# Kernel tuning notes

Measured on AMD Instinct MI355X. Metric: run time of the kernel, lower is better.

## Reference

```python
import jax, jax.numpy as jnp
import numpy as np

N, E = 20000, 320000
IN_DIM = OUT_DIM = E_IN = E_OUT = 128
BN_EPS = 1e-5

def _lrelu(x):
    return jnp.where(x >= 0, x, 0.1 * x)

def setup_inputs() -> dict:
    key = jax.random.key(0)
    ks = jax.random.split(key, 12)
    def w(k, shape):
        return jax.random.normal(k, shape, jnp.float32) * (shape[0] ** -0.5)
    return {
        "h": jax.random.normal(ks[0], (N, IN_DIM), jnp.float32),
        "edge_w": jax.random.normal(ks[1], (E, E_IN), jnp.float32),
        "W_node": w(ks[2], (IN_DIM, OUT_DIM)),
        "W_eedge": w(ks[3], (E_IN, E_IN)),
        "W_esf": w(ks[4], (E_IN, 1)),
        "W_fuse": w(ks[5], (2 * OUT_DIM + E_IN, OUT_DIM)),
        "b_fuse": jnp.zeros((OUT_DIM,), jnp.float32),
        "W_attn": w(ks[6], (OUT_DIM, 1)),
        "W_conc": w(ks[7], (2 * OUT_DIM + E_IN, OUT_DIM)),
        "b_conc": jnp.zeros((OUT_DIM,), jnp.float32),
        "bn_gamma": jnp.ones((E_IN,), jnp.float32),
        "bn_beta": jnp.zeros((E_IN,), jnp.float32),
        "W_aggre": w(ks[8], (2 * OUT_DIM + 2 * E_IN, E_OUT)),
        "src": jax.random.randint(ks[9], (E,), 0, N),
        "dst": jax.random.randint(ks[10], (E,), 0, N),
    }

def reference(h, edge_w, W_node, W_eedge, W_esf, W_fuse, b_fuse, W_attn,
              W_conc, b_conc, bn_gamma, bn_beta, W_aggre, src, dst):
    # eval mode: dropout = identity, BatchNorm uses running stats (mean 0, var 1)
    hn = h @ W_node                       # embed_node -> ndata['h'] = ndata['oh']
    # self_attention: ow = embed_edge(w); w = edge_sf_atten(lrelu(ow)) * ow
    ow = edge_w @ W_eedge                 # [E, e_in]
    w1 = (_lrelu(ow) @ W_esf) * ow        # [E, e_in]
    # inter_attention
    hs, hd = hn[src], hn[dst]             # [E, out]
    sat = jnp.concatenate([hs, hd, w1], axis=-1)          # [E, 2*out+e_in]
    inw = _lrelu(sat @ W_fuse + b_fuse)                   # [E, out]
    a = inw @ W_attn                                      # [E, 1]
    w2 = a * w1                                           # edata['w']
    # reduce_func2: segment softmax over incoming edges (grouped by dst)
    s = a[:, 0]
    m = jax.ops.segment_max(s, dst, num_segments=N)
    e = jnp.exp(s - m[dst])
    denom = jax.ops.segment_sum(e, dst, num_segments=N)
    alpha = (e / denom[dst])[:, None]                     # [E, 1]
    t = jnp.concatenate([hs, w2], axis=-1)                # [E, out+e_in]
    h_agg = jax.ops.segment_sum(alpha * t, dst, num_segments=N)  # [N, out+e_in]
    h_new = jnp.concatenate([h_agg, hn], axis=-1) @ W_conc + b_conc
    # DGL only updates nodes that received messages; zero-indegree keep embed_node(h)
    indeg = jax.ops.segment_sum(jnp.ones((E,), jnp.float32), dst, num_segments=N)
    h_out = jnp.where(indeg[:, None] > 0, h_new, hn)      # [N, out]
    # edge_calc: BN(w2) then aggre_embed_edge(cat(src_h, dst_h, bn_w, ow))
    w_bn = (w2 / jnp.sqrt(jnp.float32(1.0) + BN_EPS)) * bn_gamma + bn_beta
    z = jnp.concatenate([h_out[src], h_out[dst], w_bn, ow], axis=-1)
    w_out = z @ W_aggre                                   # [E, e_out]
    return h_out, w_out, sat
```

## Files before the change

### kernel.cpp

```cpp
#include <hip/hip_runtime.h>
#include <hip/hip_bf16.h>

#define TB 256
#define TBM 512
#define BM 64
#define BK 32
#define BN 128
#define ASTR 68
#define MAXD 160

static constexpr int NN = 20000;
static constexpr int NE = 320000;
static constexpr int NB = 313;

static constexpr long long OFF_OW  = 0;
static constexpr long long OFF_HN  = 40960000;
static constexpr long long OFF_PQ  = 43520000;
static constexpr long long OFF_S   = 48640000;
static constexpr long long OFF_DEN = 48960000;
static constexpr long long OFF_CUR = 48980000;
static constexpr long long OFF_WT  = 49000000;
static constexpr long long WS_FLOATS = 49100000;

static constexpr int U_EH = 0;
static constexpr int U_EL = 16384;
static constexpr int U_FH = 32768;
static constexpr int U_FL = 81920;
static constexpr int U_AH = 131072;
static constexpr int U_AL = 163840;

static constexpr long long OUT_HOUT = 0;
static constexpr long long OUT_WOUT = 2560000;
static constexpr long long OUT_SAT  = 43520000;

typedef __attribute__((ext_vector_type(8))) short s8v;
typedef __attribute__((ext_vector_type(4))) float f32x4;
typedef __attribute__((ext_vector_type(4))) unsigned short u16x4;

#define MFMA16(a,b,c) __builtin_amdgcn_mfma_f32_16x16x32_bf16(a,b,c,0,0,0)

__device__ __forceinline__ float lrelu(float x){ return x >= 0.f ? x : 0.1f*x; }

__device__ __forceinline__ void wsync(){ asm volatile("s_waitcnt lgkmcnt(0)" ::: "memory"); }

__device__ __forceinline__ void gl16(const void* g, void* l){
    __builtin_amdgcn_global_load_lds(
        (const __attribute__((address_space(1))) void*)g,
        (__attribute__((address_space(3))) void*)l, 16, 0, 0);
}

__device__ __forceinline__ void split1(float f, unsigned short& hi, unsigned short& lo){
    __hip_bfloat16 h = __float2bfloat16(f);
    float hf = __bfloat162float(h);
    __hip_bfloat16 l = __float2bfloat16(f - hf);
    hi = __builtin_bit_cast(unsigned short, h);
    lo = __builtin_bit_cast(unsigned short, l);
}
__device__ __forceinline__ void split8(float4 a, float4 b, s8v& hi, s8v& lo){
    float v[8] = {a.x,a.y,a.z,a.w,b.x,b.y,b.z,b.w};
#pragma unroll
    for (int j = 0; j < 8; ++j){
        unsigned short hs, ls;
        split1(v[j], hs, ls);
        hi[j] = (short)hs; lo[j] = (short)ls;
    }
}
__device__ __forceinline__ float bfp(unsigned p){
    return __uint_as_float(p & 0xffff0000u) + __uint_as_float(p << 16);
}

__device__ __forceinline__ int lds_a(int row, int g){
    return row*32 + ((g ^ (row & 3)) << 3);
}

__device__ __forceinline__ void store_At(float (*Ast)[ASTR], int k4, int r, float4 v){
    Ast[k4+0][r] = v.x; Ast[k4+1][r] = v.y; Ast[k4+2][r] = v.z; Ast[k4+3][r] = v.w;
}
__device__ __forceinline__ void mm_chunk(const float (*Ast)[ASTR], const float (*Bs)[BN],
                                         int r0, int c0, float acc[4][8]){
#pragma unroll 4
    for (int k = 0; k < BK; ++k){
        const float4 av = *(const float4*)&Ast[k][r0];
        const float4 b0 = *(const float4*)&Bs[k][c0];
        const float4 b1 = *(const float4*)&Bs[k][64 + c0];
        const float a0=av.x, a1=av.y, a2=av.z, a3=av.w;
        const float b[8] = {b0.x,b0.y,b0.z,b0.w,b1.x,b1.y,b1.z,b1.w};
#pragma unroll
        for (int j = 0; j < 8; ++j){
            acc[0][j] = fmaf(a0, b[j], acc[0][j]);
            acc[1][j] = fmaf(a1, b[j], acc[1][j]);
            acc[2][j] = fmaf(a2, b[j], acc[2][j]);
            acc[3][j] = fmaf(a3, b[j], acc[3][j]);
        }
    }
}
__device__ __forceinline__ void load_B(const float* __restrict__ W, int kc,
                                       float (*Bs)[BN], int tid){
#pragma unroll
    for (int p = 0; p < 4; ++p){
        int idx = p*TB + tid;
        int row = idx >> 5;
        int c4  = (idx & 31) << 2;
        *(float4*)&Bs[row][c4] = *(const float4*)&W[(size_t)(kc+row)*BN + c4];
    }
}

__global__ __launch_bounds__(TB) void k_prep(const float* __restrict__ We,
                                             const float* __restrict__ Wf,
                                             const float* __restrict__ Wa,
                                             unsigned short* __restrict__ wt,
                                             int* __restrict__ cur){
    int id = blockIdx.x*TB + threadIdx.x;
    if (id < NN) cur[id] = 0;
    unsigned short hs, ls;
    if (id < 16384){
        int n = id >> 7, k = id & 127;
        split1(We[(size_t)k*128 + n], hs, ls);
        wt[U_EH + id] = hs; wt[U_EL + id] = ls;
    } else if (id < 65536){
        int local = id - 16384;
        int n = local / 384, k = local - n*384;
        split1(Wf[(size_t)k*128 + n], hs, ls);
        wt[U_FH + local] = hs; wt[U_FL + local] = ls;
    } else if (id < 98304){
        int local = id - 65536;
        int n = local >> 8, kk = local & 255;
        split1(Wa[(size_t)(256+kk)*128 + n], hs, ls);
        wt[U_AH + local] = hs; wt[U_AL + local] = ls;
    }
}

__global__ __launch_bounds__(TB) void kB_count(const int* __restrict__ dst,
                                               int* __restrict__ cur){
    int e = blockIdx.x*TB + threadIdx.x;
    atomicAdd(&cur[dst[e]], 1);
}
__global__ __launch_bounds__(TB) void kC_scan(int* __restrict__ cur,
                                              int* __restrict__ offs){
    __shared__ int part[TB];
    __shared__ int spre[TB];
    const int tid = threadIdx.x;
    const int CH = (NN + TB - 1) / TB;
    const int base = tid * CH;
    int sum = 0;
    for (int i = 0; i < CH; ++i){ int idx = base + i; if (idx < NN) sum += cur[idx]; }
    part[tid] = sum;
    __syncthreads();
    if (tid == 0){ int r = 0; for (int i = 0; i < TB; ++i){ spre[i] = r; r += part[i]; } }
    __syncthreads();
    int run = spre[tid];
    for (int i = 0; i < CH; ++i){
        int idx = base + i;
        if (idx < NN){ int c = cur[idx]; offs[idx] = run; cur[idx] = run; run += c; }
    }
}
__global__ __launch_bounds__(TB) void kD_scatter(const int* __restrict__ dst,
                                                 int* __restrict__ cur,
                                                 int* __restrict__ eidx){
    int e = blockIdx.x*TB + threadIdx.x;
    int p = atomicAdd(&cur[dst[e]], 1);
    eidx[p] = e;
}

__global__ __launch_bounds__(TB) void k1_hn(const float* __restrict__ h,
                                            const float* __restrict__ Wn,
                                            unsigned short* __restrict__ hnH,
                                            unsigned short* __restrict__ hnL,
                                            unsigned* __restrict__ hnP){
    __shared__ float Ast[BK][ASTR];
    __shared__ float Bs[BK][BN];
    const int tid = threadIdx.x;
    const int rbase = blockIdx.x * BM;
    const int tc = tid & 15, tr = tid >> 4;
    const int r0 = tr*4, c0 = tc*4;
    float acc[4][8] = {};
    for (int kc = 0; kc < 128; kc += BK){
        __syncthreads();
        {
            int lr = tid >> 3, k4 = (tid & 7) << 2;
#pragma unroll
            for (int p = 0; p < 2; ++p){
                int r = p*32 + lr;
                int rr = rbase + r; if (rr >= NN) rr = NN-1;
                float4 v = *(const float4*)&h[(size_t)rr*128 + kc + k4];
                store_At(Ast, k4, r, v);
            }
        }
        load_B(Wn, kc, Bs, tid);
        __syncthreads();
        mm_chunk(Ast, Bs, r0, c0, acc);
    }
#pragma unroll
    for (int i = 0; i < 4; ++i){
        int rr = rbase + r0 + i;
        if (rr < NN){
            u16x4 h0, l0, h1, l1;
            uint4 p0, p1;
#pragma unroll
            for (int j = 0; j < 4; ++j){
                unsigned short hs, ls;
                split1(acc[i][j], hs, ls);
                h0[j] = hs; l0[j] = ls;
                ((unsigned*)&p0)[j] = ((unsigned)hs << 16) | ls;
                split1(acc[i][4+j], hs, ls);
                h1[j] = hs; l1[j] = ls;
                ((unsigned*)&p1)[j] = ((unsigned)hs << 16) | ls;
            }
            *(u16x4*)&hnH[(size_t)rr*128 + c0] = h0;
            *(u16x4*)&hnL[(size_t)rr*128 + c0] = l0;
            *(u16x4*)&hnH[(size_t)rr*128 + 64 + c0] = h1;
            *(u16x4*)&hnL[(size_t)rr*128 + 64 + c0] = l1;
            *(uint4*)&hnP[(size_t)rr*128 + c0] = p0;
            *(uint4*)&hnP[(size_t)rr*128 + 64 + c0] = p1;
        }
    }
}

__global__ __launch_bounds__(TBM) void k23_mfma(const float* __restrict__ ew,
                                                const unsigned short* __restrict__ wtEH,
                                                const unsigned short* __restrict__ wtEL,
                                                const float* __restrict__ Wesf,
                                                const unsigned short* __restrict__ wtFH,
                                                const unsigned short* __restrict__ wtFL,
                                                const float* __restrict__ bf,
                                                const float* __restrict__ Wattn,
                                                const unsigned short* __restrict__ hnH,
                                                const unsigned short* __restrict__ hnL,
                                                const unsigned* __restrict__ hnP,
                                                const int* __restrict__ src,
                                                const int* __restrict__ dst,
                                                unsigned short* __restrict__ owH,
                                                unsigned short* __restrict__ owL,
                                                float* __restrict__ sat,
                                                float* __restrict__ s_ws){
    __shared__ __align__(16) unsigned short Ah[2][4096], Al[2][4096], Bh[2][4096], Bl[2][4096];
    __shared__ float sEsf[128], sBf[128], sAtt[128];
    __shared__ int sSrc[128], sDst[128];
    const int tid = threadIdx.x;
    const long long rbase = (long long)blockIdx.x * 128;
    const int lane = tid & 63, w = tid >> 6;
    const int ls = lane & 15, lg = lane >> 4;
    const int srow = tid >> 2, sg = tid & 3;
    const int gsw = sg ^ (srow & 3);
    const int aslot = srow*32 + (gsw << 3);
    if (tid < 128){
        sEsf[tid] = Wesf[tid]; sBf[tid] = bf[tid]; sAtt[tid] = Wattn[tid];
        sSrc[tid] = src[rbase + tid]; sDst[tid] = dst[rbase + tid];
    }
    f32x4 acc1[8] = {};
    auto stageA = [&](int nb, int t){
        const int kc = t*32;
        gl16(&wtEH[srow*128 + kc + gsw*8], &Bh[nb][w*512]);
        gl16(&wtEL[srow*128 + kc + gsw*8], &Bl[nb][w*512]);
        const float* p = &ew[(rbase + srow)*128 + kc + sg*8];
        float4 v0 = *(const float4*)p, v1 = *(const float4*)(p+4);
        s8v hi, lo; split8(v0, v1, hi, lo);
        *(s8v*)&Ah[nb][aslot] = hi; *(s8v*)&Al[nb][aslot] = lo;
    };
    stageA(0, 0);
    __syncthreads();
    int cur = 0;
    for (int t = 0; t < 4; ++t){
        if (t < 3) stageA(cur^1, t+1);
        s8v ah = *(const s8v*)&Ah[cur][lds_a(w*16 + ls, lg)];
        s8v al = *(const s8v*)&Al[cur][lds_a(w*16 + ls, lg)];
#pragma unroll
        for (int ct = 0; ct < 8; ++ct){
            int c = ct*16 + ls;
            s8v bh = *(const s8v*)&Bh[cur][lds_a(c,lg)];
            s8v bl = *(const s8v*)&Bl[cur][lds_a(c,lg)];
            acc1[ct] = MFMA16(ah, bh, acc1[ct]);
            acc1[ct] = MFMA16(ah, bl, acc1[ct]);
            acc1[ct] = MFMA16(al, bh, acc1[ct]);
        }
        __syncthreads();
        cur ^= 1;
    }
    float pr[4];
#pragma unroll
    for (int reg = 0; reg < 4; ++reg){
        float p = 0.f;
#pragma unroll
        for (int ct = 0; ct < 8; ++ct)
            p += lrelu(acc1[ct][reg]) * sEsf[ct*16 + ls];
#pragma unroll
        for (int m = 1; m < 16; m <<= 1) p += __shfl_xor(p, m);
        pr[reg] = p;
        long long orow = rbase + w*16 + lg*4 + reg;
#pragma unroll
        for (int ct = 0; ct < 8; ++ct){
            float o = acc1[ct][reg];
            int col = ct*16 + ls;
            sat[orow*384 + 256 + col] = p * o;
            unsigned short hs_, ls_; split1(o, hs_, ls_);
            owH[orow*128 + col] = hs_;
            owL[orow*128 + col] = ls_;
        }
    }
    f32x4 acc2[8] = {};
    auto stageC = [&](int nb, int t2){
        const int kb = 256 + t2*32;
        gl16(&wtFH[srow*384 + kb + gsw*8], &Bh[nb][w*512]);
        gl16(&wtFL[srow*384 + kb + gsw*8], &Bl[nb][w*512]);
#pragma unroll
        for (int q = 0; q < 2; ++q){
            int ct = 2*t2 + q;
#pragma unroll
            for (int reg = 0; reg < 4; ++reg){
                int row = w*16 + lg*4 + reg;
                int col = ct*16 + ls;
                int kl = col - t2*32;
                int g = kl >> 3;
                int base = row*32 + ((g ^ (row & 3)) << 3) + (kl & 7);
                unsigned short hh, ll; split1(pr[reg] * acc1[ct][reg], hh, ll);
                Ah[nb][base] = hh;
                Al[nb][base] = ll;
            }
        }
    };
    auto stageD = [&](int nb, int t3){
        const int kc = t3*32;
        gl16(&wtFH[srow*384 + kc + gsw*8], &Bh[nb][w*512]);
        gl16(&wtFL[srow*384 + kc + gsw*8], &Bl[nb][w*512]);
        long long e = rbase + srow;
        int node = (kc < 128) ? sSrc[srow] : sDst[srow];
        int col0 = kc & 127;
        gl16(&hnH[(size_t)node*128 + col0 + gsw*8], &Ah[nb][w*512]);
        gl16(&hnL[(size_t)node*128 + col0 + gsw*8], &Al[nb][w*512]);
        const unsigned* pp = &hnP[(size_t)node*128 + col0 + sg*8];
        uint4 q0 = *(const uint4*)pp, q1 = *(const uint4*)(pp+4);
        float4 v0 = {bfp(q0.x), bfp(q0.y), bfp(q0.z), bfp(q0.w)};
        float4 v1 = {bfp(q1.x), bfp(q1.y), bfp(q1.z), bfp(q1.w)};
        *(float4*)&sat[e*384 + kc + sg*8] = v0;
        *(float4*)&sat[e*384 + kc + sg*8 + 4] = v1;
    };
    auto stage2 = [&](int nb, int u){ if (u < 4) stageC(nb, u); else stageD(nb, u - 4); };
    stage2(cur, 0);
    __syncthreads();
    for (int u = 0; u < 12; ++u){
        if (u < 11) stage2(cur^1, u+1);
        s8v ah = *(const s8v*)&Ah[cur][lds_a(w*16 + ls, lg)];
        s8v al = *(const s8v*)&Al[cur][lds_a(w*16 + ls, lg)];
#pragma unroll
        for (int ct = 0; ct < 8; ++ct){
            int c = ct*16 + ls;
            s8v bh = *(const s8v*)&Bh[cur][lds_a(c,lg)];
            s8v bl = *(const s8v*)&Bl[cur][lds_a(c,lg)];
            acc2[ct] = MFMA16(ah, bh, acc2[ct]);
            acc2[ct] = MFMA16(ah, bl, acc2[ct]);
            acc2[ct] = MFMA16(al, bh, acc2[ct]);
        }
        __syncthreads();
        cur ^= 1;
    }
#pragma unroll
    for (int reg = 0; reg < 4; ++reg){
        float p = 0.f;
#pragma unroll
        for (int ct = 0; ct < 8; ++ct){
            int col = ct*16 + ls;
            p += lrelu(acc2[ct][reg] + sBf[col]) * sAtt[col];
        }
#pragma unroll
        for (int m = 1; m < 16; m <<= 1) p += __shfl_xor(p, m);
        if (ls == 0) s_ws[rbase + w*16 + lg*4 + reg] = p;
    }
}

__global__ __launch_bounds__(TB) void k5_agg(const float* __restrict__ s,
                                             const unsigned* __restrict__ hnP,
                                             const float* __restrict__ sat,
                                             const int* __restrict__ src,
                                             const int* __restrict__ eidx,
                                             const int* __restrict__ offs,
                                             const int* __restrict__ cur,
                                             float* __restrict__ hagg,
                                             float* __restrict__ den){
    __shared__ int   sEu[4][MAXD];
    __shared__ int   sEs[4][MAXD];
    __shared__ float sAl[4][MAXD];
    __shared__ float sWc[4][MAXD];
    const int wv = threadIdx.x >> 6, lane = threadIdx.x & 63;
    const int n = blockIdx.x*4 + wv;
    int* Eu = sEu[wv]; int* Es = sEs[wv];
    float* Al = sAl[wv]; float* Wc = sWc[wv];
    const int start = offs[n];
    const int deg = cur[n] - start;
    const int dc = deg < MAXD ? deg : MAXD;
    for (int i = lane; i < dc; i += 64) Eu[i] = eidx[start+i];
    wsync();
    for (int i = lane; i < dc; i += 64){
        int my = Eu[i], r = 0;
        for (int j = 0; j < dc; ++j) r += (Eu[j] < my);
        Es[r] = my;
    }
    wsync();
    float lm = -3.402823466e38f;
    for (int i = lane; i < dc; i += 64){
        int e = Es[i];
        float sv = s[e];
        Wc[i] = sv;
        Eu[i] = src[e];
        lm = fmaxf(lm, sv);
    }
    for (int i = MAXD + lane; i < deg; i += 64) lm = fmaxf(lm, s[eidx[start+i]]);
#pragma unroll
    for (int m2 = 32; m2; m2 >>= 1) lm = fmaxf(lm, __shfl_xor(lm, m2));
    const float m = lm;
    wsync();
    float lsum = 0.f;
    for (int i = lane; i < dc; i += 64){
        float ev = expf(Wc[i] - m);
        Al[i] = ev;
        lsum += ev;
    }
    for (int i = MAXD + lane; i < deg; i += 64) lsum += expf(s[eidx[start+i]] - m);
#pragma unroll
    for (int m2 = 32; m2; m2 >>= 1) lsum += __shfl_xor(lsum, m2);
    const float denom = lsum;
    const float inv = (deg > 0) ? 1.f/denom : 0.f;
    for (int i = lane; i < dc; i += 64){
        float al = Al[i] * inv;
        Al[i] = al;
        Wc[i] = al * Wc[i];
    }
    wsync();
    float a0=0.f, a1=0.f, a2=0.f, a3=0.f;
    for (int i = 0; i < dc; ++i){
        int sI = Eu[i];
        size_t e = (size_t)Es[i];
        float al = Al[i], wc = Wc[i];
        unsigned p0 = hnP[(size_t)sI*128 + lane];
        unsigned p1 = hnP[(size_t)sI*128 + 64 + lane];
        float w0 = sat[e*384 + 256 + lane];
        float w1v = sat[e*384 + 256 + 64 + lane];
        a0 = fmaf(al, bfp(p0), a0);
        a1 = fmaf(al, bfp(p1), a1);
        a2 = fmaf(wc, w0, a2);
        a3 = fmaf(wc, w1v, a3);
    }
    for (int i = MAXD; i < deg; ++i){
        int e = eidx[start+i];
        float sv = s[e];
        float al = expf(sv - m) * inv;
        float wc = al * sv;
        int sI = src[e];
        a0 = fmaf(al, bfp(hnP[(size_t)sI*128 + lane]), a0);
        a1 = fmaf(al, bfp(hnP[(size_t)sI*128 + 64 + lane]), a1);
        a2 = fmaf(wc, sat[(size_t)e*384 + 256 + lane], a2);
        a3 = fmaf(wc, sat[(size_t)e*384 + 256 + 64 + lane], a3);
    }
    const size_t b = (size_t)n*256;
    hagg[b + lane] = a0;
    hagg[b + 64 + lane] = a1;
    hagg[b + 128 + lane] = a2;
    hagg[b + 192 + lane] = a3;
    if (lane == 0) den[n] = (deg > 0) ? denom : 0.f;
}

__global__ __launch_bounds__(TB) void k6_conc(const float* __restrict__ hagg,
                                              const unsigned* __restrict__ hnP,
                                              const float* __restrict__ Wc,
                                              const float* __restrict__ bc,
                                              const float* __restrict__ den,
                                              float* __restrict__ hout){
    __shared__ float Ast[BK][ASTR];
    __shared__ float Bs[BK][BN];
    __shared__ float sBc[BN];
    const int tid = threadIdx.x;
    const int rbase = blockIdx.x * BM;
    const int tc = tid & 15, tr = tid >> 4;
    const int r0 = tr*4, c0 = tc*4;
    if (tid < BN) sBc[tid] = bc[tid];
    float acc[4][8] = {};
    for (int chunk = 0; chunk < 12; ++chunk){
        int kc = chunk * BK;
        __syncthreads();
        {
            int lr = tid >> 3, k4 = (tid & 7) << 2;
#pragma unroll
            for (int p = 0; p < 2; ++p){
                int r = p*32 + lr;
                int rr = rbase + r; if (rr >= NN) rr = NN-1;
                float4 v;
                if (chunk < 8) v = *(const float4*)&hagg[(size_t)rr*256 + kc + k4];
                else {
                    int cb = (kc - 256) + k4;
                    uint4 q = *(const uint4*)&hnP[(size_t)rr*128 + cb];
                    v.x = bfp(q.x); v.y = bfp(q.y); v.z = bfp(q.z); v.w = bfp(q.w);
                }
                store_At(Ast, k4, r, v);
            }
        }
        load_B(Wc, kc, Bs, tid);
        __syncthreads();
        mm_chunk(Ast, Bs, r0, c0, acc);
    }
#pragma unroll
    for (int i = 0; i < 4; ++i){
        int rr = rbase + r0 + i;
        if (rr >= NN) continue;
        bool keep = den[rr] > 0.f;
        float o[8];
#pragma unroll
        for (int j = 0; j < 8; ++j){
            int col = (j < 4) ? (c0 + j) : (60 + c0 + j);
            float fb = bfp(hnP[(size_t)rr*128 + col]);
            o[j] = keep ? acc[i][j] + sBc[col] : fb;
        }
        float4 o0 = {o[0],o[1],o[2],o[3]}, o1 = {o[4],o[5],o[6],o[7]};
        *(float4*)&hout[(size_t)rr*128 + c0] = o0;
        *(float4*)&hout[(size_t)rr*128 + 64 + c0] = o1;
    }
}

__global__ __launch_bounds__(TB) void kNG(const float* __restrict__ aF,
                                          const float* __restrict__ W,
                                          float* __restrict__ O){
    __shared__ float Ast[BK][ASTR];
    __shared__ float Bs[BK][BN];
    const int tid = threadIdx.x;
    const int half = blockIdx.x >= NB ? 1 : 0;
    const int rbase = (blockIdx.x - half*NB) * BM;
    const float* Wp = W + (size_t)half*16384;
    const int tc = tid & 15, tr = tid >> 4;
    const int r0 = tr*4, c0 = tc*4;
    float acc[4][8] = {};
    for (int kc = 0; kc < 128; kc += BK){
        __syncthreads();
        {
            int lr = tid >> 3, k4 = (tid & 7) << 2;
#pragma unroll
            for (int p = 0; p < 2; ++p){
                int r = p*32 + lr;
                int rr = rbase + r; if (rr >= NN) rr = NN-1;
                float4 v = *(const float4*)&aF[(size_t)rr*128 + kc + k4];
                store_At(Ast, k4, r, v);
            }
        }
        load_B(Wp, kc, Bs, tid);
        __syncthreads();
        mm_chunk(Ast, Bs, r0, c0, acc);
    }
#pragma unroll
    for (int i = 0; i < 4; ++i){
        int rr = rbase + r0 + i;
        if (rr < NN){
            float4 o0 = {acc[i][0],acc[i][1],acc[i][2],acc[i][3]};
            float4 o1 = {acc[i][4],acc[i][5],acc[i][6],acc[i][7]};
            *(float4*)&O[(size_t)rr*256 + half*128 + c0] = o0;
            *(float4*)&O[(size_t)rr*256 + half*128 + 64 + c0] = o1;
        }
    }
}

__global__ __launch_bounds__(TBM) void k7p(const unsigned short* __restrict__ owH,
                                           const unsigned short* __restrict__ owL,
                                           const float* __restrict__ sarr,
                                           const float* __restrict__ sat,
                                           const float* __restrict__ Q,
                                           const float* __restrict__ gamma,
                                           const float* __restrict__ beta,
                                           const unsigned short* __restrict__ wtH,
                                           const unsigned short* __restrict__ wtL,
                                           const int* __restrict__ src,
                                           const int* __restrict__ dst,
                                           float* __restrict__ w2out){
    __shared__ __align__(16) unsigned short Ah[2][4096], Al[2][4096], Bh[2][4096], Bl[2][4096];
    __shared__ float sGam[128], sBet[128], sS[128];
    __shared__ int sSrc[128], sDst[128];
    const int tid = threadIdx.x;
    const long long rbase = (long long)blockIdx.x * 128;
    const int lane = tid & 63, w = tid >> 6;
    const int ls = lane & 15, lg = lane >> 4;
    const int srow = tid >> 2, sg = tid & 3;
    const int gsw = sg ^ (srow & 3);
    const int aslot = srow*32 + (gsw << 3);
    const float ISR = 0.9999950000374997f;
    if (tid < 128){
        sGam[tid] = gamma[tid] * ISR; sBet[tid] = beta[tid];
        sSrc[tid] = src[rbase + tid]; sDst[tid] = dst[rbase + tid];
        sS[tid] = sarr[rbase + tid];
    }
    __syncthreads();
    f32x4 acc[8] = {};
    auto stage = [&](int nb, int t){
        const int kc = t*32;
        gl16(&wtH[srow*256 + kc + gsw*8], &Bh[nb][w*512]);
        gl16(&wtL[srow*256 + kc + gsw*8], &Bl[nb][w*512]);
        long long e = rbase + srow;
        if (kc < 128){
            int cb = kc + sg*8;
            float se = sS[srow];
            const float* p = &sat[e*384 + 256 + cb];
            float4 v0 = *(const float4*)p, v1 = *(const float4*)(p+4);
            v0.x = fmaf(v0.x*se, sGam[cb+0], sBet[cb+0]);
            v0.y = fmaf(v0.y*se, sGam[cb+1], sBet[cb+1]);
            v0.z = fmaf(v0.z*se, sGam[cb+2], sBet[cb+2]);
            v0.w = fmaf(v0.w*se, sGam[cb+3], sBet[cb+3]);
            v1.x = fmaf(v1.x*se, sGam[cb+4], sBet[cb+4]);
            v1.y = fmaf(v1.y*se, sGam[cb+5], sBet[cb+5]);
            v1.z = fmaf(v1.z*se, sGam[cb+6], sBet[cb+6]);
            v1.w = fmaf(v1.w*se, sGam[cb+7], sBet[cb+7]);
            s8v hi, lo; split8(v0, v1, hi, lo);
            *(s8v*)&Ah[nb][aslot] = hi; *(s8v*)&Al[nb][aslot] = lo;
        } else {
            int col0 = kc - 128;
            gl16(&owH[e*128 + col0 + gsw*8], &Ah[nb][w*512]);
            gl16(&owL[e*128 + col0 + gsw*8], &Al[nb][w*512]);
        }
    };
    stage(0, 0);
    __syncthreads();
    int cur = 0;
    for (int t = 0; t < 8; ++t){
        if (t+1 < 8) stage(cur^1, t+1);
        int r = w*16 + ls;
        s8v ah = *(const s8v*)&Ah[cur][r*32 + ((lg ^ (r&3)) << 3)];
        s8v al = *(const s8v*)&Al[cur][r*32 + ((lg ^ (r&3)) << 3)];
#pragma unroll
        for (int ct = 0; ct < 8; ++ct){
            int c = ct*16 + ls;
            s8v bh = *(const s8v*)&Bh[cur][c*32 + ((lg ^ (c&3)) << 3)];
            s8v bl = *(const s8v*)&Bl[cur][c*32 + ((lg ^ (c&3)) << 3)];
            acc[ct] = MFMA16(ah, bh, acc[ct]);
            acc[ct] = MFMA16(ah, bl, acc[ct]);
            acc[ct] = MFMA16(al, bh, acc[ct]);
        }
        __syncthreads();
        cur ^= 1;
    }
#pragma unroll
    for (int reg = 0; reg < 4; ++reg){
        int row = w*16 + lg*4 + reg;
        long long orow = rbase + row;
        int sI = sSrc[row], dI = sDst[row];
#pragma unroll
        for (int ct = 0; ct < 8; ++ct){
            int col = ct*16 + ls;
            w2out[orow*128 + col] = acc[ct][reg]
                                  + Q[(size_t)sI*256 + col]
                                  + Q[(size_t)dI*256 + 128 + col];
        }
    }
}

extern "C" void kernel_launch(void* const* d_in, const int* in_sizes, int n_in,
                              void* d_out, int out_size, void* d_ws, size_t ws_size,
                              hipStream_t stream){
    (void)in_sizes; (void)n_in; (void)out_size;
    const float* h       = (const float*)d_in[0];
    const float* edge_w  = (const float*)d_in[1];
    const float* W_node  = (const float*)d_in[2];
    const float* W_eedge = (const float*)d_in[3];
    const float* W_esf   = (const float*)d_in[4];
    const float* W_fuse  = (const float*)d_in[5];
    const float* b_fuse  = (const float*)d_in[6];
    const float* W_attn  = (const float*)d_in[7];
    const float* W_conc  = (const float*)d_in[8];
    const float* b_conc  = (const float*)d_in[9];
    const float* gamma   = (const float*)d_in[10];
    const float* beta    = (const float*)d_in[11];
    const float* W_aggre = (const float*)d_in[12];
    const int*   src     = (const int*)d_in[13];
    const int*   dst     = (const int*)d_in[14];

    float* out    = (float*)d_out;
    float* o_hout = out + OUT_HOUT;
    float* o_wout = out + OUT_WOUT;
    float* o_sat  = out + OUT_SAT;

    if (ws_size < (size_t)WS_FLOATS * 4) return;
    float* ws     = (float*)d_ws;
    unsigned short* w_owH = (unsigned short*)(ws + OFF_OW);
    unsigned short* w_owL = w_owH + (size_t)NE*128;
    unsigned short* w_hnH = (unsigned short*)(ws + OFF_HN);
    unsigned short* w_hnL = w_hnH + (size_t)NN*128;
    float* w_PQ   = ws + OFF_PQ;
    float* w_s    = ws + OFF_S;
    float* w_den  = ws + OFF_DEN;
    int*   w_cur  = (int*)(ws + OFF_CUR);
    unsigned short* w_wt = (unsigned short*)(ws + OFF_WT);

    unsigned* w_hnP = (unsigned*)o_wout;
    int* w_eidx = (int*)o_hout;
    int* w_offs = w_eidx + NE;

    hipLaunchKernelGGL(k_prep,    dim3(98304/TB), dim3(TB), 0, stream,
                       W_eedge, W_fuse, W_aggre, w_wt, w_cur);
    hipLaunchKernelGGL(kB_count,  dim3(NE/TB), dim3(TB), 0, stream, dst, w_cur);
    hipLaunchKernelGGL(kC_scan,   dim3(1), dim3(TB), 0, stream, w_cur, w_offs);
    hipLaunchKernelGGL(kD_scatter,dim3(NE/TB), dim3(TB), 0, stream, dst, w_cur, w_eidx);
    hipLaunchKernelGGL(k1_hn,     dim3(NB), dim3(TB), 0, stream, h, W_node,
                       w_hnH, w_hnL, w_hnP);
    hipLaunchKernelGGL(k23_mfma,  dim3(NE/128), dim3(TBM), 0, stream, edge_w,
                       w_wt + U_EH, w_wt + U_EL, W_esf,
                       w_wt + U_FH, w_wt + U_FL, b_fuse, W_attn,
                       w_hnH, w_hnL, w_hnP, src, dst,
                       w_owH, w_owL, o_sat, w_s);
    hipLaunchKernelGGL(k5_agg,    dim3(NN/4), dim3(TB), 0, stream, w_s, w_hnP, o_sat,
                       src, w_eidx, w_offs, w_cur, w_PQ, w_den);
    hipLaunchKernelGGL(k6_conc,   dim3(NB), dim3(TB), 0, stream, w_PQ,
                       w_hnP, W_conc, b_conc, w_den, o_hout);
    hipLaunchKernelGGL(kNG,       dim3(2*NB), dim3(TB), 0, stream, o_hout, W_aggre, w_PQ);
    hipLaunchKernelGGL(k7p,       dim3(NE/128), dim3(TBM), 0, stream,
                       w_owH, w_owL, w_s, o_sat, w_PQ, gamma, beta,
                       w_wt + U_AH, w_wt + U_AL, src, dst, o_wout);
}
```

Measured before the change: 698.9 us.

## Fuse node-side W_aggre projection into k6_conc, prefetch aggregation loads, add nontemporal stores

Removes the separate kNG kernel. k6_conc now keeps its h_out tile in registers, restages it through shared memory and computes the two W_aggre node projections (Q) directly, so h_out is not re-read from global memory and one launch disappears. The k5 aggregation loop gets one-step software prefetching of the gathered hn and sat values to hide gather latency. The large sat and w_out outputs are written with nontemporal stores to reduce cache pollution. The fused kernel reads hagg and writes Q into the same buffer under __restrict__, which is only safe because each block touches just its own rows; the restaging also adds extra syncs and register pressure.

```diff
diff --git a/kernel.cpp b/kernel.cpp
--- a/kernel.cpp
+++ b/kernel.cpp
@@ -329,10 +329,10 @@
         gl16(&hnL[(size_t)node*128 + col0 + gsw*8], &Al[nb][w*512]);
         const unsigned* pp = &hnP[(size_t)node*128 + col0 + sg*8];
         uint4 q0 = *(const uint4*)pp, q1 = *(const uint4*)(pp+4);
-        float4 v0 = {bfp(q0.x), bfp(q0.y), bfp(q0.z), bfp(q0.w)};
-        float4 v1 = {bfp(q1.x), bfp(q1.y), bfp(q1.z), bfp(q1.w)};
-        *(float4*)&sat[e*384 + kc + sg*8] = v0;
-        *(float4*)&sat[e*384 + kc + sg*8 + 4] = v1;
+        f32x4 v0 = {bfp(q0.x), bfp(q0.y), bfp(q0.z), bfp(q0.w)};
+        f32x4 v1 = {bfp(q1.x), bfp(q1.y), bfp(q1.z), bfp(q1.w)};
+        __builtin_nontemporal_store(v0, (f32x4*)&sat[e*384 + kc + sg*8]);
+        __builtin_nontemporal_store(v1, (f32x4*)&sat[e*384 + kc + sg*8 + 4]);
     };
     auto stage2 = [&](int nb, int u){ if (u < 4) stageC(nb, u); else stageD(nb, u - 4); };
     stage2(cur, 0);
@@ -426,18 +426,29 @@
     }
     wsync();
     float a0=0.f, a1=0.f, a2=0.f, a3=0.f;
+    unsigned p0n=0, p1n=0; float w0n=0.f, w1n=0.f;
+    if (dc > 0){
+        int sI = Eu[0]; size_t e0 = (size_t)Es[0];
+        p0n = hnP[(size_t)sI*128 + lane];
+        p1n = hnP[(size_t)sI*128 + 64 + lane];
+        w0n = sat[e0*384 + 256 + lane];
+        w1n = sat[e0*384 + 256 + 64 + lane];
+    }
     for (int i = 0; i < dc; ++i){
-        int sI = Eu[i];
-        size_t e = (size_t)Es[i];
+        unsigned p0c = p0n, p1c = p1n;
+        float w0c = w0n, w1c = w1n;
         float al = Al[i], wc = Wc[i];
-        unsigned p0 = hnP[(size_t)sI*128 + lane];
-        unsigned p1 = hnP[(size_t)sI*128 + 64 + lane];
-        float w0 = sat[e*384 + 256 + lane];
-        float w1v = sat[e*384 + 256 + 64 + lane];
-        a0 = fmaf(al, bfp(p0), a0);
-        a1 = fmaf(al, bfp(p1), a1);
-        a2 = fmaf(wc, w0, a2);
-        a3 = fmaf(wc, w1v, a3);
+        if (i+1 < dc){
+            int sI = Eu[i+1]; size_t e1 = (size_t)Es[i+1];
+            p0n = hnP[(size_t)sI*128 + lane];
+            p1n = hnP[(size_t)sI*128 + 64 + lane];
+            w0n = sat[e1*384 + 256 + lane];
+            w1n = sat[e1*384 + 256 + 64 + lane];
+        }
+        a0 = fmaf(al, bfp(p0c), a0);
+        a1 = fmaf(al, bfp(p1c), a1);
+        a2 = fmaf(wc, w0c, a2);
+        a3 = fmaf(wc, w1c, a3);
     }
     for (int i = MAXD; i < deg; ++i){
         int e = eidx[start+i];
@@ -463,7 +474,9 @@
                                               const float* __restrict__ Wc,
                                               const float* __restrict__ bc,
                                               const float* __restrict__ den,
-                                              float* __restrict__ hout){
+                                              const float* __restrict__ Wa,
+                                              float* __restrict__ hout,
+                                              float* __restrict__ Q){
     __shared__ float Ast[BK][ASTR];
     __shared__ float Bs[BK][BN];
     __shared__ float sBc[BN];
@@ -496,60 +509,62 @@
         __syncthreads();
         mm_chunk(Ast, Bs, r0, c0, acc);
     }
+    float ho[4][8];
 #pragma unroll
     for (int i = 0; i < 4; ++i){
         int rr = rbase + r0 + i;
-        if (rr >= NN) continue;
-        bool keep = den[rr] > 0.f;
-        float o[8];
+        int rc = rr < NN ? rr : NN-1;
+        bool keep = den[rc] > 0.f;
 #pragma unroll
         for (int j = 0; j < 8; ++j){
             int col = (j < 4) ? (c0 + j) : (60 + c0 + j);
-            float fb = bfp(hnP[(size_t)rr*128 + col]);
-            o[j] = keep ? acc[i][j] + sBc[col] : fb;
-        }
-        float4 o0 = {o[0],o[1],o[2],o[3]}, o1 = {o[4],o[5],o[6],o[7]};
-        *(float4*)&hout[(size_t)rr*128 + c0] = o0;
-        *(float4*)&hout[(size_t)rr*128 + 64 + c0] = o1;
-    }
-}
-
-__global__ __launch_bounds__(TB) void kNG(const float* __restrict__ aF,
-                                          const float* __restrict__ W,
-                                          float* __restrict__ O){
-    __shared__ float Ast[BK][ASTR];
-    __shared__ float Bs[BK][BN];
-    const int tid = threadIdx.x;
-    const int half = blockIdx.x >= NB ? 1 : 0;
-    const int rbase = (blockIdx.x - half*NB) * BM;
-    const float* Wp = W + (size_t)half*16384;
-    const int tc = tid & 15, tr = tid >> 4;
-    const int r0 = tr*4, c0 = tc*4;
-    float acc[4][8] = {};
-    for (int kc = 0; kc < 128; kc += BK){
-        __syncthreads();
-        {
-            int lr = tid >> 3, k4 = (tid & 7) << 2;
-#pragma unroll
-            for (int p = 0; p < 2; ++p){
-                int r = p*32 + lr;
-                int rr = rbase + r; if (rr >= NN) rr = NN-1;
-                float4 v = *(const float4*)&aF[(size_t)rr*128 + kc + k4];
-                store_At(Ast, k4, r, v);
+            float fb = bfp(hnP[(size_t)rc*128 + col]);
+            ho[i][j] = keep ? acc[i][j] + sBc[col] : fb;
+        }
+        if (rr < NN){
+            float4 o0 = {ho[i][0],ho[i][1],ho[i][2],ho[i][3]};
+            float4 o1 = {ho[i][4],ho[i][5],ho[i][6],ho[i][7]};
+            *(float4*)&hout[(size_t)rr*128 + c0] = o0;
+            *(float4*)&hout[(size_t)rr*128 + 64 + c0] = o1;
+        }
+    }
+#pragma unroll
+    for (int half = 0; half < 2; ++half){
+        float accQ[4][8] = {};
+        const float* Wp = Wa + (size_t)half*16384;
+        for (int chunk = 0; chunk < 4; ++chunk){
+            int kc = chunk*32;
+            __syncthreads();
+            if (kc < 64){
+                if (c0 >= kc && c0 < kc+32){
+#pragma unroll
+                    for (int j = 0; j < 4; ++j)
+#pragma unroll
+                        for (int i = 0; i < 4; ++i)
+                            Ast[c0 + j - kc][r0 + i] = ho[i][j];
+                }
+            } else {
+                if (c0 >= kc-64 && c0 < kc-32){
+#pragma unroll
+                    for (int j = 0; j < 4; ++j)
+#pragma unroll
+                        for (int i = 0; i < 4; ++i)
+                            Ast[64 + c0 + j - kc][r0 + i] = ho[i][4+j];
+                }
             }
-        }
-        load_B(Wp, kc, Bs, tid);
-        __syncthreads();
-        mm_chunk(Ast, Bs, r0, c0, acc);
-    }
-#pragma unroll
-    for (int i = 0; i < 4; ++i){
-        int rr = rbase + r0 + i;
-        if (rr < NN){
-            float4 o0 = {acc[i][0],acc[i][1],acc[i][2],acc[i][3]};
-            float4 o1 = {acc[i][4],acc[i][5],acc[i][6],acc[i][7]};
-            *(float4*)&O[(size_t)rr*256 + half*128 + c0] = o0;
-            *(float4*)&O[(size_t)rr*256 + half*128 + 64 + c0] = o1;
+            load_B(Wp, kc, Bs, tid);
+            __syncthreads();
+            mm_chunk(Ast, Bs, r0, c0, accQ);
+        }
+#pragma unroll
+        for (int i = 0; i < 4; ++i){
+            int rr = rbase + r0 + i;
+            if (rr < NN){
+                float4 o0 = {accQ[i][0],accQ[i][1],accQ[i][2],accQ[i][3]};
+                float4 o1 = {accQ[i][4],accQ[i][5],accQ[i][6],accQ[i][7]};
+                *(float4*)&Q[(size_t)rr*256 + half*128 + c0] = o0;
+                *(float4*)&Q[(size_t)rr*256 + half*128 + 64 + c0] = o1;
+            }
         }
     }
 }
@@ -638,9 +653,10 @@
 #pragma unroll
         for (int ct = 0; ct < 8; ++ct){
             int col = ct*16 + ls;
-            w2out[orow*128 + col] = acc[ct][reg]
-                                  + Q[(size_t)sI*256 + col]
-                                  + Q[(size_t)dI*256 + 128 + col];
+            float v = acc[ct][reg]
+                    + Q[(size_t)sI*256 + col]
+                    + Q[(size_t)dI*256 + 128 + col];
+            __builtin_nontemporal_store(v, &w2out[orow*128 + col]);
         }
     }
 }
@@ -701,8 +717,7 @@
     hipLaunchKernelGGL(k5_agg,    dim3(NN/4), dim3(TB), 0, stream, w_s, w_hnP, o_sat,
                        src, w_eidx, w_offs, w_cur, w_PQ, w_den);
     hipLaunchKernelGGL(k6_conc,   dim3(NB), dim3(TB), 0, stream, w_PQ,
-                       w_hnP, W_conc, b_conc, w_den, o_hout);
-    hipLaunchKernelGGL(kNG,       dim3(2*NB), dim3(TB), 0, stream, o_hout, W_aggre, w_PQ);
+                       w_hnP, W_conc, b_conc, w_den, W_aggre, o_hout, w_PQ);
     hipLaunchKernelGGL(k7p,       dim3(NE/128), dim3(TBM), 0, stream,
                        w_owH, w_owL, w_s, o_sat, w_PQ, gamma, beta,
                        w_wt + U_AH, w_wt + U_AL, src, dst, o_wout);
```

Measured after the change: 706.4 us. No clear change (+1.1%).

## Fuse edge-aggregation GEMM into edge kernel, folding BatchNorm into weights

Applied to the files above, without the earlier changes.

The w_bn/ow part of the W_aggre product now runs inside k23_mfma while ow is still in registers. The edge tile is split to bf16 hi/lo directly into LDS, so ow no longer goes to a global hi/lo workspace and is not reloaded. BatchNorm scale is folded into the weights and beta into a bias vector. The per-edge s*a factor is applied as one fma on a separately accumulated partial product. A light elementwise kernel then adds the gathered per-node Q terms. This trades the ow write/read and the separate k7p GEMM for an fp32 partial write plus a streaming add pass, with more registers held in k23.

```diff
diff --git a/kernel.cpp b/kernel.cpp
--- a/kernel.cpp
+++ b/kernel.cpp
@@ -13,21 +13,24 @@
 static constexpr int NE = 320000;
 static constexpr int NB = 313;
 
-static constexpr long long OFF_OW  = 0;
+static constexpr long long OFF_WP  = 0;
 static constexpr long long OFF_HN  = 40960000;
 static constexpr long long OFF_PQ  = 43520000;
 static constexpr long long OFF_S   = 48640000;
 static constexpr long long OFF_DEN = 48960000;
 static constexpr long long OFF_CUR = 48980000;
 static constexpr long long OFF_WT  = 49000000;
+static constexpr long long OFF_BV  = 49050000;
 static constexpr long long WS_FLOATS = 49100000;
 
-static constexpr int U_EH = 0;
-static constexpr int U_EL = 16384;
-static constexpr int U_FH = 32768;
-static constexpr int U_FL = 81920;
-static constexpr int U_AH = 131072;
-static constexpr int U_AL = 163840;
+static constexpr int U_EH  = 0;
+static constexpr int U_EL  = 16384;
+static constexpr int U_FH  = 32768;
+static constexpr int U_FL  = 81920;
+static constexpr int U_AaH = 131072;
+static constexpr int U_AaL = 147456;
+static constexpr int U_AbH = 163840;
+static constexpr int U_AbL = 180224;
 
 static constexpr long long OUT_HOUT = 0;
 static constexpr long long OUT_WOUT = 2560000;
@@ -108,10 +111,12 @@
 __global__ __launch_bounds__(TB) void k_prep(const float* __restrict__ We,
                                              const float* __restrict__ Wf,
                                              const float* __restrict__ Wa,
+                                             const float* __restrict__ gamma,
                                              unsigned short* __restrict__ wt,
                                              int* __restrict__ cur){
     int id = blockIdx.x*TB + threadIdx.x;
     if (id < NN) cur[id] = 0;
+    const float ISR = 0.9999950000374997f;
     unsigned short hs, ls;
     if (id < 16384){
         int n = id >> 7, k = id & 127;
@@ -122,12 +127,27 @@
         int n = local / 384, k = local - n*384;
         split1(Wf[(size_t)k*128 + n], hs, ls);
         wt[U_FH + local] = hs; wt[U_FL + local] = ls;
+    } else if (id < 81920){
+        int local = id - 65536;
+        int n = local >> 7, k = local & 127;
+        split1(ISR * gamma[k] * Wa[(size_t)(256+k)*128 + n], hs, ls);
+        wt[U_AaH + local] = hs; wt[U_AaL + local] = ls;
     } else if (id < 98304){
-        int local = id - 65536;
-        int n = local >> 8, kk = local & 255;
-        split1(Wa[(size_t)(256+kk)*128 + n], hs, ls);
-        wt[U_AH + local] = hs; wt[U_AL + local] = ls;
-    }
+        int local = id - 81920;
+        int n = local >> 7, k = local & 127;
+        split1(Wa[(size_t)(384+k)*128 + n], hs, ls);
+        wt[U_AbH + local] = hs; wt[U_AbL + local] = ls;
+    }
+}
+
+__global__ __launch_bounds__(128) void kBV(const float* __restrict__ beta,
+                                           const float* __restrict__ Wa,
+                                           float* __restrict__ bvec){
+    int n = threadIdx.x;
+    float acc = 0.f;
+    for (int k = 0; k < 128; ++k)
+        acc = fmaf(beta[k], Wa[(size_t)(256+k)*128 + n], acc);
+    bvec[n] = acc;
 }
 
 __global__ __launch_bounds__(TB) void kB_count(const int* __restrict__ dst,
@@ -224,17 +244,21 @@
                                                 const unsigned short* __restrict__ wtFL,
                                                 const float* __restrict__ bf,
                                                 const float* __restrict__ Wattn,
+                                                const unsigned short* __restrict__ wtAaH,
+                                                const unsigned short* __restrict__ wtAaL,
+                                                const unsigned short* __restrict__ wtAbH,
+                                                const unsigned short* __restrict__ wtAbL,
+                                                const float* __restrict__ bvec,
                                                 const unsigned short* __restrict__ hnH,
                                                 const unsigned short* __restrict__ hnL,
                                                 const unsigned* __restrict__ hnP,
                                                 const int* __restrict__ src,
                                                 const int* __restrict__ dst,
-                                                unsigned short* __restrict__ owH,
-                                                unsigned short* __restrict__ owL,
+                                                float* __restrict__ wpart,
                                                 float* __restrict__ sat,
                                                 float* __restrict__ s_ws){
     __shared__ __align__(16) unsigned short Ah[2][4096], Al[2][4096], Bh[2][4096], Bl[2][4096];
-    __shared__ float sEsf[128], sBf[128], sAtt[128];
+    __shared__ float sEsf[128], sBf[128], sAtt[128], sBv[128];
     __shared__ int sSrc[128], sDst[128];
     const int tid = threadIdx.x;
     const long long rbase = (long long)blockIdx.x * 128;
@@ -245,6 +269,7 @@
     const int aslot = srow*32 + (gsw << 3);
     if (tid < 128){
         sEsf[tid] = Wesf[tid]; sBf[tid] = bf[tid]; sAtt[tid] = Wattn[tid];
+        sBv[tid] = bvec[tid];
         sSrc[tid] = src[rbase + tid]; sDst[tid] = dst[rbase + tid];
     }
     f32x4 acc1[8] = {};
@@ -288,14 +313,8 @@
         pr[reg] = p;
         long long orow = rbase + w*16 + lg*4 + reg;
 #pragma unroll
-        for (int ct = 0; ct < 8; ++ct){
-            float o = acc1[ct][reg];
-            int col = ct*16 + ls;
-            sat[orow*384 + 256 + col] = p * o;
-            unsigned short hs_, ls_; split1(o, hs_, ls_);
-            owH[orow*128 + col] = hs_;
-            owL[orow*128 + col] = ls_;
-        }
+        for (int ct = 0; ct < 8; ++ct)
+            sat[orow*384 + 256 + ct*16 + ls] = p * acc1[ct][reg];
     }
     f32x4 acc2[8] = {};
     auto stageC = [&](int nb, int t2){
@@ -353,6 +372,7 @@
         __syncthreads();
         cur ^= 1;
     }
+    float sv[4];
 #pragma unroll
     for (int reg = 0; reg < 4; ++reg){
         float p = 0.f;
@@ -363,7 +383,60 @@
         }
 #pragma unroll
         for (int m = 1; m < 16; m <<= 1) p += __shfl_xor(p, m);
+        sv[reg] = p;
         if (ls == 0) s_ws[rbase + w*16 + lg*4 + reg] = p;
+    }
+    f32x4 accG1[8] = {}, accG2[8] = {};
+    auto stageG = [&](int nb, int u){
+        int t2 = u & 3;
+        const unsigned short* BH = (u < 4) ? wtAaH : wtAbH;
+        const unsigned short* BL = (u < 4) ? wtAaL : wtAbL;
+        gl16(&BH[srow*128 + t2*32 + gsw*8], &Bh[nb][w*512]);
+        gl16(&BL[srow*128 + t2*32 + gsw*8], &Bl[nb][w*512]);
+#pragma unroll
+        for (int q = 0; q < 2; ++q){
+            int ct = 2*t2 + q;
+#pragma unroll
+            for (int reg = 0; reg < 4; ++reg){
+                int row = w*16 + lg*4 + reg;
+                int col = ct*16 + ls;
+                int kl = col - t2*32;
+                int g = kl >> 3;
+                int base = row*32 + ((g ^ (row & 3)) << 3) + (kl & 7);
+                unsigned short hh, ll; split1(acc1[ct][reg], hh, ll);
+                Ah[nb][base] = hh;
+                Al[nb][base] = ll;
+            }
+        }
+    };
+    stageG(cur, 0);
+    __syncthreads();
+    for (int u = 0; u < 8; ++u){
+        if (u < 7) stageG(cur^1, u+1);
+        s8v ah = *(const s8v*)&Ah[cur][lds_a(w*16 + ls, lg)];
+        s8v al = *(const s8v*)&Al[cur][lds_a(w*16 + ls, lg)];
+        f32x4* acg = (u < 4) ? accG1 : accG2;
+#pragma unroll
+        for (int ct = 0; ct < 8; ++ct){
+            int c = ct*16 + ls;
+            s8v bh = *(const s8v*)&Bh[cur][lds_a(c,lg)];
+            s8v bl = *(const s8v*)&Bl[cur][lds_a(c,lg)];
+            acg[ct] = MFMA16(ah, bh, acg[ct]);
+            acg[ct] = MFMA16(ah, bl, acg[ct]);
+            acg[ct] = MFMA16(al, bh, acg[ct]);
+        }
+        __syncthreads();
+        cur ^= 1;
+    }
+#pragma unroll
+    for (int reg = 0; reg < 4; ++reg){
+        float c_ = pr[reg] * sv[reg];
+        long long orow = rbase + w*16 + lg*4 + reg;
+#pragma unroll
+        for (int ct = 0; ct < 8; ++ct){
+            int col = ct*16 + ls;
+            wpart[orow*128 + col] = fmaf(c_, accG1[ct][reg], accG2[ct][reg]) + sBv[col];
+        }
     }
 }
 
@@ -554,95 +627,21 @@
     }
 }
 
-__global__ __launch_bounds__(TBM) void k7p(const unsigned short* __restrict__ owH,
-                                           const unsigned short* __restrict__ owL,
-                                           const float* __restrict__ sarr,
-                                           const float* __restrict__ sat,
-                                           const float* __restrict__ Q,
-                                           const float* __restrict__ gamma,
-                                           const float* __restrict__ beta,
-                                           const unsigned short* __restrict__ wtH,
-                                           const unsigned short* __restrict__ wtL,
-                                           const int* __restrict__ src,
-                                           const int* __restrict__ dst,
-                                           float* __restrict__ w2out){
-    __shared__ __align__(16) unsigned short Ah[2][4096], Al[2][4096], Bh[2][4096], Bl[2][4096];
-    __shared__ float sGam[128], sBet[128], sS[128];
-    __shared__ int sSrc[128], sDst[128];
-    const int tid = threadIdx.x;
-    const long long rbase = (long long)blockIdx.x * 128;
-    const int lane = tid & 63, w = tid >> 6;
-    const int ls = lane & 15, lg = lane >> 4;
-    const int srow = tid >> 2, sg = tid & 3;
-    const int gsw = sg ^ (srow & 3);
-    const int aslot = srow*32 + (gsw << 3);
-    const float ISR = 0.9999950000374997f;
-    if (tid < 128){
-        sGam[tid] = gamma[tid] * ISR; sBet[tid] = beta[tid];
-        sSrc[tid] = src[rbase + tid]; sDst[tid] = dst[rbase + tid];
-        sS[tid] = sarr[rbase + tid];
-    }
-    __syncthreads();
-    f32x4 acc[8] = {};
-    auto stage = [&](int nb, int t){
-        const int kc = t*32;
-        gl16(&wtH[srow*256 + kc + gsw*8], &Bh[nb][w*512]);
-        gl16(&wtL[srow*256 + kc + gsw*8], &Bl[nb][w*512]);
-        long long e = rbase + srow;
-        if (kc < 128){
-            int cb = kc + sg*8;
-            float se = sS[srow];
-            const float* p = &sat[e*384 + 256 + cb];
-            float4 v0 = *(const float4*)p, v1 = *(const float4*)(p+4);
-            v0.x = fmaf(v0.x*se, sGam[cb+0], sBet[cb+0]);
-            v0.y = fmaf(v0.y*se, sGam[cb+1], sBet[cb+1]);
-            v0.z = fmaf(v0.z*se, sGam[cb+2], sBet[cb+2]);
-            v0.w = fmaf(v0.w*se, sGam[cb+3], sBet[cb+3]);
-            v1.x = fmaf(v1.x*se, sGam[cb+4], sBet[cb+4]);
-            v1.y = fmaf(v1.y*se, sGam[cb+5], sBet[cb+5]);
-            v1.z = fmaf(v1.z*se, sGam[cb+6], sBet[cb+6]);
-            v1.w = fmaf(v1.w*se, sGam[cb+7], sBet[cb+7]);
-            s8v hi, lo; split8(v0, v1, hi, lo);
-            *(s8v*)&Ah[nb][aslot] = hi; *(s8v*)&Al[nb][aslot] = lo;
-        } else {
-            int col0 = kc - 128;
-            gl16(&owH[e*128 + col0 + gsw*8], &Ah[nb][w*512]);
-            gl16(&owL[e*128 + col0 + gsw*8], &Al[nb][w*512]);
-        }
-    };
-    stage(0, 0);
-    __syncthreads();
-    int cur = 0;
-    for (int t = 0; t < 8; ++t){
-        if (t+1 < 8) stage(cur^1, t+1);
-        int r = w*16 + ls;
-        s8v ah = *(const s8v*)&Ah[cur][r*32 + ((lg ^ (r&3)) << 3)];
-        s8v al = *(const s8v*)&Al[cur][r*32 + ((lg ^ (r&3)) << 3)];
-#pragma unroll
-        for (int ct = 0; ct < 8; ++ct){
-            int c = ct*16 + ls;
-            s8v bh = *(const s8v*)&Bh[cur][c*32 + ((lg ^ (c&3)) << 3)];
-            s8v bl = *(const s8v*)&Bl[cur][c*32 + ((lg ^ (c&3)) << 3)];
-            acc[ct] = MFMA16(ah, bh, acc[ct]);
-            acc[ct] = MFMA16(ah, bl, acc[ct]);
-            acc[ct] = MFMA16(al, bh, acc[ct]);
-        }
-        __syncthreads();
-        cur ^= 1;
-    }
-#pragma unroll
-    for (int reg = 0; reg < 4; ++reg){
-        int row = w*16 + lg*4 + reg;
-        long long orow = rbase + row;
-        int sI = sSrc[row], dI = sDst[row];
-#pragma unroll
-        for (int ct = 0; ct < 8; ++ct){
-            int col = ct*16 + ls;
-            w2out[orow*128 + col] = acc[ct][reg]
-                                  + Q[(size_t)sI*256 + col]
-                                  + Q[(size_t)dI*256 + 128 + col];
-        }
-    }
+__global__ __launch_bounds__(TB) void kWO(const float* __restrict__ wpart,
+                                          const float* __restrict__ Q,
+                                          const int* __restrict__ src,
+                                          const int* __restrict__ dst,
+                                          float* __restrict__ wout){
+    int idx = blockIdx.x*TB + threadIdx.x;
+    int e = idx >> 5;
+    int c4 = (idx & 31) << 2;
+    int sI = src[e], dI = dst[e];
+    float4 a = *(const float4*)&wpart[(size_t)e*128 + c4];
+    float4 qs = *(const float4*)&Q[(size_t)sI*256 + c4];
+    float4 qd = *(const float4*)&Q[(size_t)dI*256 + 128 + c4];
+    float4 o = {a.x + qs.x + qd.x, a.y + qs.y + qd.y,
+                a.z + qs.z + qd.z, a.w + qs.w + qd.w};
+    *(float4*)&wout[(size_t)e*128 + c4] = o;
 }
 
 extern "C" void kernel_launch(void* const* d_in, const int* in_sizes, int n_in,
@@ -672,8 +671,7 @@
 
     if (ws_size < (size_t)WS_FLOATS * 4) return;
     float* ws     = (float*)d_ws;
-    unsigned short* w_owH = (unsigned short*)(ws + OFF_OW);
-    unsigned short* w_owL = w_owH + (size_t)NE*128;
+    float* w_wp   = ws + OFF_WP;
     unsigned short* w_hnH = (unsigned short*)(ws + OFF_HN);
     unsigned short* w_hnL = w_hnH + (size_t)NN*128;
     float* w_PQ   = ws + OFF_PQ;
@@ -681,13 +679,15 @@
     float* w_den  = ws + OFF_DEN;
     int*   w_cur  = (int*)(ws + OFF_CUR);
     unsigned short* w_wt = (unsigned short*)(ws + OFF_WT);
+    float* w_bv   = ws + OFF_BV;
 
     unsigned* w_hnP = (unsigned*)o_wout;
     int* w_eidx = (int*)o_hout;
     int* w_offs = w_eidx + NE;
 
     hipLaunchKernelGGL(k_prep,    dim3(98304/TB), dim3(TB), 0, stream,
-                       W_eedge, W_fuse, W_aggre, w_wt, w_cur);
+                       W_eedge, W_fuse, W_aggre, gamma, w_wt, w_cur);
+    hipLaunchKernelGGL(kBV,       dim3(1), dim3(128), 0, stream, beta, W_aggre, w_bv);
     hipLaunchKernelGGL(kB_count,  dim3(NE/TB), dim3(TB), 0, stream, dst, w_cur);
     hipLaunchKernelGGL(kC_scan,   dim3(1), dim3(TB), 0, stream, w_cur, w_offs);
     hipLaunchKernelGGL(kD_scatter,dim3(NE/TB), dim3(TB), 0, stream, dst, w_cur, w_eidx);
@@ -696,14 +696,14 @@
     hipLaunchKernelGGL(k23_mfma,  dim3(NE/128), dim3(TBM), 0, stream, edge_w,
                        w_wt + U_EH, w_wt + U_EL, W_esf,
                        w_wt + U_FH, w_wt + U_FL, b_fuse, W_attn,
+                       w_wt + U_AaH, w_wt + U_AaL, w_wt + U_AbH, w_wt + U_AbL, w_bv,
                        w_hnH, w_hnL, w_hnP, src, dst,
-                       w_owH, w_owL, o_sat, w_s);
+                       w_wp, o_sat, w_s);
     hipLaunchKernelGGL(k5_agg,    dim3(NN/4), dim3(TB), 0, stream, w_s, w_hnP, o_sat,
                        src, w_eidx, w_offs, w_cur, w_PQ, w_den);
     hipLaunchKernelGGL(k6_conc,   dim3(NB), dim3(TB), 0, stream, w_PQ,
                        w_hnP, W_conc, b_conc, w_den, o_hout);
     hipLaunchKernelGGL(kNG,       dim3(2*NB), dim3(TB), 0, stream, o_hout, W_aggre, w_PQ);
-    hipLaunchKernelGGL(k7p,       dim3(NE/128), dim3(TBM), 0, stream,
-                       w_owH, w_owL, w_s, o_sat, w_PQ, gamma, beta,
-                       w_wt + U_AH, w_wt + U_AL, src, dst, o_wout);
-}
+    hipLaunchKernelGGL(kWO,       dim3(NE*32/TB), dim3(TB), 0, stream,
+                       w_wp, w_PQ, src, dst, o_wout);
+}
```

Result: slower. 718.2 us (+2.8%).
